# Kernel tuning notes

Measured on AMD Instinct MI355X. Metric: run time of the kernel, lower is better.

## Reference

```python
import jax, jax.numpy as jnp
import numpy as np

B, P, Q, N, D = 64, 12, 12, 1024, 64
DOW, TOD = 7, 288  # day-of-week / time-of-day one-hot depths (GMAN STEmbedding)


def setup_inputs() -> dict:
    key = jax.random.key(0)
    ks = iter(jax.random.split(key, 40))
    def g(shape, scale=0.05):
        return jax.random.normal(next(ks), shape, jnp.float32) * scale
    inp = {
        "X": jax.random.normal(next(ks), (B, P, N), jnp.float32),
        "ZC": jax.random.normal(next(ks), (B, P, 400), jnp.float32),
        "ZF": jax.random.normal(next(ks), (B, P, 1600), jnp.float32),
        "SE": g((N, D)),
        # STEmbedding FCs
        "W_se1": g((D, D)), "b_se1": jnp.zeros((D,), jnp.float32),
        "W_se2": g((D, D)), "b_se2": jnp.zeros((D,), jnp.float32),
        "W_te1": g((DOW + TOD, D)), "b_te1": jnp.zeros((D,), jnp.float32),
        "W_te2": g((D, D)), "b_te2": jnp.zeros((D,), jnp.float32),
        # FC_X_in
        "W_in1": g((1, D)), "b_in1": jnp.zeros((D,), jnp.float32),
        "W_in2": g((D, D)), "b_in2": jnp.zeros((D,), jnp.float32),
        # DCGRU layer 1 (gconv over [x||state, support@(x||state)] -> 4D input)
        "Wg1": g((4 * D, 2 * D)), "bg1": jnp.ones((2 * D,), jnp.float32),
        "Wc1": g((4 * D, D)), "bc1": jnp.zeros((D,), jnp.float32),
        # DCGRU layer 2
        "Wg2": g((4 * D, 2 * D)), "bg2": jnp.ones((2 * D,), jnp.float32),
        "Wc2": g((4 * D, D)), "bc2": jnp.zeros((D,), jnp.float32),
        # FC_X_out
        "W_o1": g((D, D)), "b_o1": jnp.zeros((D,), jnp.float32),
        "W_o2": g((D, Q)), "b_o2": jnp.zeros((Q,), jnp.float32),
        "TE": jax.random.randint(next(ks), (B, P + Q, 2), 0, 7, jnp.int32),
    }
    return inp


def _dcgru_scan(x_seq, support, Wg, bg, Wc, bc):
    """x_seq: [B,P,N,D] -> (sequence [B,P,N,D], last state [B,N,D])."""
    def gconv(x, s, W, b):
        z = jnp.concatenate([x, s], -1)                      # [B,N,2D]
        z1 = jnp.einsum('nm,bmd->bnd', support, z)           # diffusion step K=1
        return jnp.concatenate([z, z1], -1) @ W + b

    def step(state, x_t):
        ru = jax.nn.sigmoid(gconv(x_t, state, Wg, bg))       # [B,N,2D]
        r, u = jnp.split(ru, 2, axis=-1)
        c = jnp.tanh(gconv(x_t, r * state, Wc, bc))
        new = u * state + (1.0 - u) * c
        return new, new

    state0 = jnp.zeros(x_seq.shape[:1] + x_seq.shape[2:], x_seq.dtype)
    last, seq = jax.lax.scan(step, state0, jnp.swapaxes(x_seq, 0, 1))
    return jnp.swapaxes(seq, 0, 1), last


def reference(X, ZC, ZF, SE, W_se1, b_se1, W_se2, b_se2, W_te1, b_te1,
              W_te2, b_te2, W_in1, b_in1, W_in2, b_in2,
              Wg1, bg1, Wc1, bc1, Wg2, bg2, Wc2, bc2,
              W_o1, b_o1, W_o2, b_o2, TE):
    # adjacency is identity in this module; random_walk(I).T == I
    adj = jnp.eye(N, dtype=jnp.float32)
    support = (adj / jnp.sum(adj, axis=1, keepdims=True)).T

    # STEmbedding: spatial + temporal embedding
    se = jax.nn.relu(SE @ W_se1 + b_se1) @ W_se2 + b_se2                 # [N,D]
    te_oh = jnp.concatenate([
        jax.nn.one_hot(TE[..., 0], DOW, dtype=jnp.float32),
        jax.nn.one_hot(TE[..., 1], TOD, dtype=jnp.float32)], -1)        # [B,P+Q,295]
    te = jax.nn.relu(te_oh @ W_te1 + b_te1) @ W_te2 + b_te2              # [B,P+Q,D]
    STEX = (se[None, None] + te[:, :, None, :])[:, :P]                   # [B,P,N,D]

    # FC_X_in on expanded X, add STE
    Xe = X[..., None]                                                    # [B,P,N,1]
    Xe = jax.nn.relu(Xe @ W_in1 + b_in1) @ W_in2 + b_in2                 # [B,P,N,D]
    Xe = Xe + STEX

    seq1, _ = _dcgru_scan(Xe, support, Wg1, bg1, Wc1, bc1)               # [B,P,N,D]
    _, h = _dcgru_scan(seq1, support, Wg2, bg2, Wc2, bc2)                # [B,N,D]

    Y = jax.nn.relu(h @ W_o1 + b_o1) @ W_o2 + b_o2                       # [B,N,Q]
    return jnp.transpose(Y, (0, 2, 1))                                   # [B,Q,N]
```

## Files before the change

kernel.cpp:

```cpp
#include <hip/hip_runtime.h>


#define NB 1024

typedef float f32x4 __attribute__((ext_vector_type(4)));
typedef __bf16 bf16x8 __attribute__((ext_vector_type(8)));
typedef int i32x4 __attribute__((ext_vector_type(4)));
typedef unsigned int u32;
typedef unsigned short u16;

#define MFMA(a, b, c) __builtin_amdgcn_mfma_f32_16x16x32_bf16(a, b, c, 0, 0, 0)

__device__ __forceinline__ float fexp(float x) {
    return __builtin_amdgcn_exp2f(x * 1.44269504088896341f);
}
__device__ __forceinline__ float fsigmoid(float x) {
    return __builtin_amdgcn_rcpf(1.0f + fexp(-x));
}
__device__ __forceinline__ float ftanh(float x) {
    return 1.0f - 2.0f * __builtin_amdgcn_rcpf(1.0f + fexp(2.0f * x));
}

__device__ __forceinline__ u32 packf(float v) {
    u32 u = __builtin_bit_cast(u32, v);
    u32 hb = u & 0xFFFF0000u;
    float lo = v - __builtin_bit_cast(float, hb);
    return hb | (__builtin_bit_cast(u32, lo) >> 16);
}
__device__ __forceinline__ float unpackf(u32 u) {
    return __builtin_bit_cast(float, u & 0xFFFF0000u)
         + __builtin_bit_cast(float, u << 16);
}

__device__ __forceinline__ bf16x8 ldfrag(const u16* p) {
    i32x4 t = *(const i32x4*)p;
    return __builtin_bit_cast(bf16x8, t);
}
__device__ __forceinline__ bf16x8 pin(bf16x8 v) {
    i32x4 t = __builtin_bit_cast(i32x4, v);
    asm volatile("" : "+v"(t));
    return __builtin_bit_cast(bf16x8, t);
}
__device__ __forceinline__ void split8(f32x4 a0, f32x4 a1, bf16x8& hi, bf16x8& lo) {
    #pragma unroll
    for (int i = 0; i < 4; i++) {
        __bf16 h0 = (__bf16)a0[i]; hi[i] = h0;     lo[i] = (__bf16)(a0[i] - (float)h0);
        __bf16 h1 = (__bf16)a1[i]; hi[4 + i] = h1; lo[4 + i] = (__bf16)(a1[i] - (float)h1);
    }
}

#define SWZ(t) ((((t) & 3) << 3) ^ ((t) & 4) ^ (((t) & 8) << 1))
#define SW(t, k) ((t) * 64 + ((k) ^ SWZ(t)))

__device__ __forceinline__ void lda_packed(const u32* __restrict__ src, int m, int kk,
                                           bf16x8& hi, bf16x8& lo) {
    const int sk = kk ^ SWZ(m);
    i32x4 d0 = *(const i32x4*)(src + m * 64 + sk);
    i32x4 d1 = *(const i32x4*)(src + m * 64 + (sk ^ 4));
    i32x4 h, L;
    h[0] = (int)__builtin_amdgcn_perm((u32)d0[1], (u32)d0[0], 0x07060302u);
    h[1] = (int)__builtin_amdgcn_perm((u32)d0[3], (u32)d0[2], 0x07060302u);
    h[2] = (int)__builtin_amdgcn_perm((u32)d1[1], (u32)d1[0], 0x07060302u);
    h[3] = (int)__builtin_amdgcn_perm((u32)d1[3], (u32)d1[2], 0x07060302u);
    L[0] = (int)__builtin_amdgcn_perm((u32)d0[1], (u32)d0[0], 0x05040100u);
    L[1] = (int)__builtin_amdgcn_perm((u32)d0[3], (u32)d0[2], 0x05040100u);
    L[2] = (int)__builtin_amdgcn_perm((u32)d1[1], (u32)d1[0], 0x05040100u);
    L[3] = (int)__builtin_amdgcn_perm((u32)d1[3], (u32)d1[2], 0x05040100u);
    hi = __builtin_bit_cast(bf16x8, h);
    lo = __builtin_bit_cast(bf16x8, L);
}


__device__ __forceinline__ void wsplit(float v, u16* dhi, u16* dlo) {
    __bf16 h = (__bf16)v;
    __bf16 l = (__bf16)(v - (float)h);
    *dhi = __builtin_bit_cast(u16, h);
    *dlo = __builtin_bit_cast(u16, l);
}

__global__ void prep_gates(const float* __restrict__ Wg1, const float* __restrict__ Wg2,
                           u16* __restrict__ fr) {
    int i = blockIdx.x * 256 + threadIdx.x;
    if (i >= 4096) return;
    int layer = i >> 11, r = i & 2047;
    int w = r >> 9; r &= 511; int nt = r >> 8; r &= 255; int ks = r >> 6; int lane = r & 63;
    const float* Wg = layer ? Wg2 : Wg1;
    int n = lane & 15, q = lane >> 4;
    int col = nt ? (64 + w * 16 + n) : (w * 16 + n);
    u16* dst = fr + layer * 32768 + (((w * 2 + nt) * 4 + ks) * 2) * 512 + lane * 8;
    #pragma unroll
    for (int j = 0; j < 8; j++) {
        int k = ks * 32 + q * 8 + j;
        float v = Wg[k * 128 + col] + Wg[(k + 128) * 128 + col];
        wsplit(v, dst + j, dst + 512 + j);
    }
}

__global__ void prep_cand(const float* __restrict__ Wc1, const float* __restrict__ Wc2,
                          u16* __restrict__ fr) {
    int i = blockIdx.x * 256 + threadIdx.x;
    if (i >= 2048) return;
    int layer = i >> 10, r = i & 1023;
    int w = r >> 8; r &= 255; int ks = r >> 6; int lane = r & 63;
    const float* Wc = layer ? Wc2 : Wc1;
    int n = lane & 15, q = lane >> 4;
    int col = w * 16 + n;
    u16* dst = fr + 65536 + layer * 16384 + ((w * 4 + ks) * 2) * 512 + lane * 8;
    #pragma unroll
    for (int j = 0; j < 8; j++) {
        int k = ks * 32 + q * 8 + j;
        float v = Wc[k * 64 + col] + Wc[(k + 128) * 64 + col];
        wsplit(v, dst + j, dst + 512 + j);
    }
}

__global__ void prep_small(const float* __restrict__ Win2, const float* __restrict__ Wo1,
                           u16* __restrict__ fr) {
    int i = blockIdx.x * 256 + threadIdx.x;
    if (i >= 1024) return;
    int kind = i >> 9, r = i & 511;
    int w = r >> 7; r &= 127; int ks = r >> 6; int lane = r & 63;
    const float* W = kind ? Wo1 : Win2;
    int n = lane & 15, q = lane >> 4;
    int col = w * 16 + n;
    u16* dst = fr + 98304 + kind * 8192 + ((w * 2 + ks) * 2) * 512 + lane * 8;
    #pragma unroll
    for (int j = 0; j < 8; j++) {
        int k = ks * 32 + q * 8 + j;
        float v = W[k * 64 + col];
        wsplit(v, dst + j, dst + 512 + j);
    }
}

__global__ void prep_se(const float* __restrict__ SE, const float* __restrict__ W1,
                        const float* __restrict__ b1, const float* __restrict__ W2,
                        const float* __restrict__ b2, const float* __restrict__ bin2,
                        float* __restrict__ seB) {
    __shared__ float h[64];
    int n = blockIdx.x, d = threadIdx.x;
    float acc = b1[d];
    for (int k = 0; k < 64; k++) acc = fmaf(SE[n * 64 + k], W1[k * 64 + d], acc);
    h[d] = fmaxf(acc, 0.0f);
    __syncthreads();
    float acc2 = b2[d];
    for (int k = 0; k < 64; k++) acc2 = fmaf(h[k], W2[k * 64 + d], acc2);
    int nb = n >> 6, tok = n & 63;
    int mt = tok >> 4, q = (tok >> 2) & 3, r = tok & 3;
    int w = d >> 4, n16 = d & 15;
    seB[(((nb * 4 + w) * 64) + q * 16 + n16) * 16 + mt * 4 + r] = acc2 + bin2[d];
}

__global__ void prep_te(const int* __restrict__ TE, const float* __restrict__ W1,
                        const float* __restrict__ b1, const float* __restrict__ W2,
                        const float* __restrict__ b2, float* __restrict__ teo) {
    __shared__ float h[64];
    int bp = blockIdx.x;
    int b = bp / 12, p = bp - b * 12;
    int d = threadIdx.x;
    int dow = TE[(b * 24 + p) * 2 + 0];
    int tod = TE[(b * 24 + p) * 2 + 1];
    float v = W1[dow * 64 + d] + W1[(7 + tod) * 64 + d] + b1[d];
    h[d] = fmaxf(v, 0.0f);
    __syncthreads();
    float acc = b2[d];
    for (int k = 0; k < 64; k++) acc = fmaf(h[k], W2[k * 64 + d], acc);
    teo[bp * 64 + d] = acc;
}

__device__ __forceinline__ void gru_full(
    const u32* __restrict__ XIN, u32* __restrict__ S, u32* __restrict__ RS,
    const bf16x8 (&g)[16], const u16* __restrict__ frC,
    float bgr, float bgu, float bcc, int l, int col) {
    const int n16 = l & 15, q = l >> 4;
    f32x4 accR[4], accU[4], accC[4];
    #pragma unroll
    for (int mt = 0; mt < 4; mt++) {
        accR[mt] = (f32x4)0.0f; accU[mt] = (f32x4)0.0f; accC[mt] = (f32x4)0.0f;
    }
    #pragma unroll
    for (int ks = 0; ks < 2; ks++) {
        bf16x8 bhiC = ldfrag(frC + (ks * 2 + 0) * 512 + l * 8);
        bf16x8 bloC = ldfrag(frC + (ks * 2 + 1) * 512 + l * 8);
        const int kk = ks * 32 + q * 8;
        #pragma unroll
        for (int mt = 0; mt < 4; mt++) {
            bf16x8 ahi, alo;
            lda_packed(XIN, mt * 16 + n16, kk, ahi, alo);
            accR[mt] = MFMA(ahi, g[ks * 2 + 0], accR[mt]);
            accR[mt] = MFMA(alo, g[ks * 2 + 0], accR[mt]);
            accR[mt] = MFMA(ahi, g[ks * 2 + 1], accR[mt]);
            accU[mt] = MFMA(ahi, g[8 + ks * 2 + 0], accU[mt]);
            accU[mt] = MFMA(alo, g[8 + ks * 2 + 0], accU[mt]);
            accU[mt] = MFMA(ahi, g[8 + ks * 2 + 1], accU[mt]);
            accC[mt] = MFMA(ahi, bhiC, accC[mt]);
            accC[mt] = MFMA(alo, bhiC, accC[mt]);
            accC[mt] = MFMA(ahi, bloC, accC[mt]);
        }
    }
    #pragma unroll
    for (int ks = 2; ks < 4; ks++) {
        const int kk = (ks - 2) * 32 + q * 8;
        #pragma unroll
        for (int mt = 0; mt < 4; mt++) {
            bf16x8 ahi, alo;
            lda_packed(S, mt * 16 + n16, kk, ahi, alo);
            accR[mt] = MFMA(ahi, g[ks * 2 + 0], accR[mt]);
            accR[mt] = MFMA(alo, g[ks * 2 + 0], accR[mt]);
            accR[mt] = MFMA(ahi, g[ks * 2 + 1], accR[mt]);
            accU[mt] = MFMA(ahi, g[8 + ks * 2 + 0], accU[mt]);
            accU[mt] = MFMA(alo, g[8 + ks * 2 + 0], accU[mt]);
            accU[mt] = MFMA(ahi, g[8 + ks * 2 + 1], accU[mt]);
        }
    }
    float soldv[16];
    #pragma unroll
    for (int mt = 0; mt < 4; mt++)
        #pragma unroll
        for (int r = 0; r < 4; r++) {
            int tok = mt * 16 + q * 4 + r;
            int a = SW(tok, col);
            float sold = unpackf(S[a]);
            soldv[mt * 4 + r] = sold;
            RS[a] = packf(fsigmoid(accR[mt][r] + bgr) * sold);
        }
    __syncthreads();
    #pragma unroll
    for (int ks = 2; ks < 4; ks++) {
        bf16x8 bhi = ldfrag(frC + (ks * 2 + 0) * 512 + l * 8);
        bf16x8 blo = ldfrag(frC + (ks * 2 + 1) * 512 + l * 8);
        const int kk = (ks - 2) * 32 + q * 8;
        #pragma unroll
        for (int mt = 0; mt < 4; mt++) {
            bf16x8 ahi, alo;
            lda_packed(RS, mt * 16 + n16, kk, ahi, alo);
            accC[mt] = MFMA(ahi, bhi, accC[mt]);
            accC[mt] = MFMA(alo, bhi, accC[mt]);
            accC[mt] = MFMA(ahi, blo, accC[mt]);
        }
    }
    #pragma unroll
    for (int mt = 0; mt < 4; mt++)
        #pragma unroll
        for (int r = 0; r < 4; r++) {
            int tok = mt * 16 + q * 4 + r;
            int a = SW(tok, col);
            float u = fsigmoid(accU[mt][r] + bgu);
            float cnd = ftanh(accC[mt][r] + bcc);
            S[a] = packf(u * soldv[mt * 4 + r] + (1.0f - u) * cnd);
        }
    __syncthreads();
}

__global__ __launch_bounds__(256, 2) void gman_main(
    const float* __restrict__ X, const float* __restrict__ ws,
    const float* __restrict__ Win1, const float* __restrict__ bin1,
    const float* __restrict__ bg1, const float* __restrict__ bc1,
    const float* __restrict__ bg2, const float* __restrict__ bc2,
    const float* __restrict__ bo1, const float* __restrict__ Wo2,
    const float* __restrict__ bo2, float* __restrict__ out) {
    __shared__ u32 XE[4096], S1[4096], S2[4096], RS[4096];

    const int tid = threadIdx.x;
    const int l = tid & 63;
    const int w = tid >> 6;
    const int uw = __builtin_amdgcn_readfirstlane(w);
    const int n16 = l & 15, q = l >> 4;
    const int col = uw * 16 + n16;
    const int b = blockIdx.x >> 4;
    const int nb = blockIdx.x & 15;
    const int n0 = nb << 6;

    const u16* frU = (const u16*)ws;
    const u16* frG1 = frU + uw * 8192;
    const u16* frG2 = frU + 32768 + uw * 8192;
    const u16* frC1 = frU + 65536 + uw * 4096;
    const u16* frC2 = frU + 81920 + uw * 4096;
    const u16* frX  = frU + 98304 + uw * 2048;
    const u16* frH  = frU + 106496 + uw * 2048;
    const float* seQ = ws + 57344 + (((nb * 4 + uw) * 64) + l) * 16;
    const float* teo = ws + 122880;

    #pragma unroll
    for (int i = 0; i < 16; i++) { S1[tid + i * 256] = 0u; S2[tid + i * 256] = 0u; }

    bf16x8 g1[16], g2[16];
    #pragma unroll
    for (int i = 0; i < 16; i++) g1[i] = pin(ldfrag(frG1 + i * 512 + l * 8));
    #pragma unroll
    for (int i = 0; i < 16; i++) g2[i] = pin(ldfrag(frG2 + i * 512 + l * 8));

    f32x4 se_v[4];
    #pragma unroll
    for (int mt = 0; mt < 4; mt++) se_v[mt] = *(const f32x4*)(seQ + mt * 4);
    const float bg1r = bg1[col], bg1u = bg1[64 + col], bc1c = bc1[col];
    const float bg2r = bg2[col], bg2u = bg2[64 + col], bc2c = bc2[col];

    #pragma unroll 1
    for (int p = 0; p < 12; p++) {
        if (tid < 64) RS[tid] = __builtin_bit_cast(u32, X[(b * 12 + p) * NB + n0 + tid]);
        __syncthreads();
        f32x4 accX[4];
        #pragma unroll
        for (int mt = 0; mt < 4; mt++) accX[mt] = (f32x4)0.0f;
        #pragma unroll
        for (int ks = 0; ks < 2; ks++) {
            const int k0 = ks * 32 + q * 8;
            f32x4 w1a = *(const f32x4*)(Win1 + k0), w1b = *(const f32x4*)(Win1 + k0 + 4);
            f32x4 b1a = *(const f32x4*)(bin1 + k0), b1b = *(const f32x4*)(bin1 + k0 + 4);
            bf16x8 bhi = ldfrag(frX + (ks * 2 + 0) * 512 + l * 8);
            bf16x8 blo = ldfrag(frX + (ks * 2 + 1) * 512 + l * 8);
            #pragma unroll
            for (int mt = 0; mt < 4; mt++) {
                const float xm = __builtin_bit_cast(float, RS[mt * 16 + n16]);
                f32x4 h0, h1v;
                #pragma unroll
                for (int i = 0; i < 4; i++) {
                    h0[i]  = fmaxf(fmaf(xm, w1a[i], b1a[i]), 0.0f);
                    h1v[i] = fmaxf(fmaf(xm, w1b[i], b1b[i]), 0.0f);
                }
                bf16x8 ahi, alo; split8(h0, h1v, ahi, alo);
                accX[mt] = MFMA(ahi, bhi, accX[mt]);
                accX[mt] = MFMA(alo, bhi, accX[mt]);
                accX[mt] = MFMA(ahi, blo, accX[mt]);
            }
        }
        const float tev = teo[(b * 12 + p) * 64 + col];
        __syncthreads();
        #pragma unroll
        for (int mt = 0; mt < 4; mt++)
            #pragma unroll
            for (int r = 0; r < 4; r++) {
                int tok = mt * 16 + q * 4 + r;
                XE[SW(tok, col)] = packf(accX[mt][r] + se_v[mt][r] + tev);
            }
        __syncthreads();

        gru_full(XE, S1, RS, g1, frC1, bg1r, bg1u, bc1c, l, col);
        gru_full(S1, S2, RS, g2, frC2, bg2r, bg2u, bc2c, l, col);
    }

    f32x4 accH[4];
    #pragma unroll
    for (int mt = 0; mt < 4; mt++) accH[mt] = (f32x4)0.0f;
    #pragma unroll
    for (int ks = 0; ks < 2; ks++) {
        bf16x8 bhi = ldfrag(frH + (ks * 2 + 0) * 512 + l * 8);
        bf16x8 blo = ldfrag(frH + (ks * 2 + 1) * 512 + l * 8);
        const int kk = ks * 32 + q * 8;
        #pragma unroll
        for (int mt = 0; mt < 4; mt++) {
            bf16x8 ahi, alo;
            lda_packed(S2, mt * 16 + n16, kk, ahi, alo);
            accH[mt] = MFMA(ahi, bhi, accH[mt]);
            accH[mt] = MFMA(alo, bhi, accH[mt]);
            accH[mt] = MFMA(ahi, blo, accH[mt]);
        }
    }
    const float bo1c = bo1[col];
    #pragma unroll
    for (int mt = 0; mt < 4; mt++)
        #pragma unroll
        for (int r = 0; r < 4; r++) {
            int tok = mt * 16 + q * 4 + r;
            XE[SW(tok, col)] = packf(fmaxf(accH[mt][r] + bo1c, 0.0f));
        }
    __syncthreads();
    const int swzt = SWZ(l);
    float y0 = bo2[3 * uw + 0], y1 = bo2[3 * uw + 1], y2 = bo2[3 * uw + 2];
    #pragma unroll
    for (int c = 0; c < 16; c++) {
        i32x4 d = *(const i32x4*)(XE + l * 64 + c * 4);
        const int j0 = (c * 4) ^ swzt;
        #pragma unroll
        for (int e = 0; e < 4; e++) {
            float hj = unpackf((u32)d[e]);
            int j = j0 + e;
            y0 = fmaf(hj, Wo2[j * 12 + 3 * uw + 0], y0);
            y1 = fmaf(hj, Wo2[j * 12 + 3 * uw + 1], y1);
            y2 = fmaf(hj, Wo2[j * 12 + 3 * uw + 2], y2);
        }
    }
    out[(b * 12 + 3 * uw + 0) * NB + n0 + l] = y0;
    out[(b * 12 + 3 * uw + 1) * NB + n0 + l] = y1;
    out[(b * 12 + 3 * uw + 2) * NB + n0 + l] = y2;
}

extern "C" void kernel_launch(void* const* d_in, const int* in_sizes, int n_in,
                              void* d_out, int out_size, void* d_ws, size_t ws_size,
                              hipStream_t stream) {
    const float* X    = (const float*)d_in[0];
    const float* SE   = (const float*)d_in[3];
    const float* Wse1 = (const float*)d_in[4];
    const float* bse1 = (const float*)d_in[5];
    const float* Wse2 = (const float*)d_in[6];
    const float* bse2 = (const float*)d_in[7];
    const float* Wte1 = (const float*)d_in[8];
    const float* bte1 = (const float*)d_in[9];
    const float* Wte2 = (const float*)d_in[10];
    const float* bte2 = (const float*)d_in[11];
    const float* Win1 = (const float*)d_in[12];
    const float* bin1 = (const float*)d_in[13];
    const float* Win2 = (const float*)d_in[14];
    const float* bin2 = (const float*)d_in[15];
    const float* Wg1  = (const float*)d_in[16];
    const float* bg1  = (const float*)d_in[17];
    const float* Wc1  = (const float*)d_in[18];
    const float* bc1  = (const float*)d_in[19];
    const float* Wg2  = (const float*)d_in[20];
    const float* bg2  = (const float*)d_in[21];
    const float* Wc2  = (const float*)d_in[22];
    const float* bc2  = (const float*)d_in[23];
    const float* Wo1  = (const float*)d_in[24];
    const float* bo1  = (const float*)d_in[25];
    const float* Wo2  = (const float*)d_in[26];
    const float* bo2  = (const float*)d_in[27];
    const int*   TE   = (const int*)d_in[28];

    float* ws = (float*)d_ws;
    u16* fr = (u16*)ws;
    float* seB = ws + 57344;
    float* teo = ws + 122880;
    float* out = (float*)d_out;

    prep_gates<<<16, 256, 0, stream>>>(Wg1, Wg2, fr);
    prep_cand<<<8, 256, 0, stream>>>(Wc1, Wc2, fr);
    prep_small<<<4, 256, 0, stream>>>(Win2, Wo1, fr);
    prep_se<<<1024, 64, 0, stream>>>(SE, Wse1, bse1, Wse2, bse2, bin2, seB);
    prep_te<<<768, 64, 0, stream>>>(TE, Wte1, bte1, Wte2, bte2, teo);
    gman_main<<<1024, 256, 0, stream>>>(X, ws, Win1, bin1, bg1, bc1, bg2, bc2,
                                        bo1, Wo2, bo2, out);
}
```

Baseline: 574.8 us.

## Stream gate weights from memory and drop RS buffer to fit three blocks per CU

Gate weight fragments are no longer held in registers for the whole kernel. They are reloaded from global memory inside each GRU step, and old state values are re-read from LDS instead of being kept in registers. The separate RS shared buffer is removed by aliasing it onto XE, with an extra barrier in the first layer, and launch bounds are raised to 3 blocks per CU. This trades repeated global/L2 weight loads and one more sync for lower register and LDS use, aiming for higher occupancy to hide latency.

```diff
diff --git a/kernel.cpp b/kernel.cpp
--- a/kernel.cpp
+++ b/kernel.cpp
@@ -34,11 +34,6 @@
 
 __device__ __forceinline__ bf16x8 ldfrag(const u16* p) {
     i32x4 t = *(const i32x4*)p;
-    return __builtin_bit_cast(bf16x8, t);
-}
-__device__ __forceinline__ bf16x8 pin(bf16x8 v) {
-    i32x4 t = __builtin_bit_cast(i32x4, v);
-    asm volatile("" : "+v"(t));
     return __builtin_bit_cast(bf16x8, t);
 }
 __device__ __forceinline__ void split8(f32x4 a0, f32x4 a1, bf16x8& hi, bf16x8& lo) {
@@ -167,9 +162,10 @@
     teo[bp * 64 + d] = acc;
 }
 
+template <bool ALIAS>
 __device__ __forceinline__ void gru_full(
     const u32* __restrict__ XIN, u32* __restrict__ S, u32* __restrict__ RS,
-    const bf16x8 (&g)[16], const u16* __restrict__ frC,
+    const u16* __restrict__ frG, const u16* __restrict__ frC,
     float bgr, float bgu, float bcc, int l, int col) {
     const int n16 = l & 15, q = l >> 4;
     f32x4 accR[4], accU[4], accC[4];
@@ -179,6 +175,10 @@
     }
     #pragma unroll
     for (int ks = 0; ks < 2; ks++) {
+        bf16x8 gRh = ldfrag(frG + (ks * 2 + 0) * 512 + l * 8);
+        bf16x8 gRl = ldfrag(frG + (ks * 2 + 1) * 512 + l * 8);
+        bf16x8 gUh = ldfrag(frG + (8 + ks * 2 + 0) * 512 + l * 8);
+        bf16x8 gUl = ldfrag(frG + (8 + ks * 2 + 1) * 512 + l * 8);
         bf16x8 bhiC = ldfrag(frC + (ks * 2 + 0) * 512 + l * 8);
         bf16x8 bloC = ldfrag(frC + (ks * 2 + 1) * 512 + l * 8);
         const int kk = ks * 32 + q * 8;
@@ -186,12 +186,12 @@
         for (int mt = 0; mt < 4; mt++) {
             bf16x8 ahi, alo;
             lda_packed(XIN, mt * 16 + n16, kk, ahi, alo);
-            accR[mt] = MFMA(ahi, g[ks * 2 + 0], accR[mt]);
-            accR[mt] = MFMA(alo, g[ks * 2 + 0], accR[mt]);
-            accR[mt] = MFMA(ahi, g[ks * 2 + 1], accR[mt]);
-            accU[mt] = MFMA(ahi, g[8 + ks * 2 + 0], accU[mt]);
-            accU[mt] = MFMA(alo, g[8 + ks * 2 + 0], accU[mt]);
-            accU[mt] = MFMA(ahi, g[8 + ks * 2 + 1], accU[mt]);
+            accR[mt] = MFMA(ahi, gRh, accR[mt]);
+            accR[mt] = MFMA(alo, gRh, accR[mt]);
+            accR[mt] = MFMA(ahi, gRl, accR[mt]);
+            accU[mt] = MFMA(ahi, gUh, accU[mt]);
+            accU[mt] = MFMA(alo, gUh, accU[mt]);
+            accU[mt] = MFMA(ahi, gUl, accU[mt]);
             accC[mt] = MFMA(ahi, bhiC, accC[mt]);
             accC[mt] = MFMA(alo, bhiC, accC[mt]);
             accC[mt] = MFMA(ahi, bloC, accC[mt]);
@@ -199,29 +199,31 @@
     }
     #pragma unroll
     for (int ks = 2; ks < 4; ks++) {
+        bf16x8 gRh = ldfrag(frG + (ks * 2 + 0) * 512 + l * 8);
+        bf16x8 gRl = ldfrag(frG + (ks * 2 + 1) * 512 + l * 8);
+        bf16x8 gUh = ldfrag(frG + (8 + ks * 2 + 0) * 512 + l * 8);
+        bf16x8 gUl = ldfrag(frG + (8 + ks * 2 + 1) * 512 + l * 8);
         const int kk = (ks - 2) * 32 + q * 8;
         #pragma unroll
         for (int mt = 0; mt < 4; mt++) {
             bf16x8 ahi, alo;
             lda_packed(S, mt * 16 + n16, kk, ahi, alo);
-            accR[mt] = MFMA(ahi, g[ks * 2 + 0], accR[mt]);
-            accR[mt] = MFMA(alo, g[ks * 2 + 0], accR[mt]);
-            accR[mt] = MFMA(ahi, g[ks * 2 + 1], accR[mt]);
-            accU[mt] = MFMA(ahi, g[8 + ks * 2 + 0], accU[mt]);
-            accU[mt] = MFMA(alo, g[8 + ks * 2 + 0], accU[mt]);
-            accU[mt] = MFMA(ahi, g[8 + ks * 2 + 1], accU[mt]);
-        }
-    }
-    float soldv[16];
+            accR[mt] = MFMA(ahi, gRh, accR[mt]);
+            accR[mt] = MFMA(alo, gRh, accR[mt]);
+            accR[mt] = MFMA(ahi, gRl, accR[mt]);
+            accU[mt] = MFMA(ahi, gUh, accU[mt]);
+            accU[mt] = MFMA(alo, gUh, accU[mt]);
+            accU[mt] = MFMA(ahi, gUl, accU[mt]);
+        }
+    }
+    if (ALIAS) __syncthreads();
     #pragma unroll
     for (int mt = 0; mt < 4; mt++)
         #pragma unroll
         for (int r = 0; r < 4; r++) {
             int tok = mt * 16 + q * 4 + r;
             int a = SW(tok, col);
-            float sold = unpackf(S[a]);
-            soldv[mt * 4 + r] = sold;
-            RS[a] = packf(fsigmoid(accR[mt][r] + bgr) * sold);
+            RS[a] = packf(fsigmoid(accR[mt][r] + bgr) * unpackf(S[a]));
         }
     __syncthreads();
     #pragma unroll
@@ -246,19 +248,20 @@
             int a = SW(tok, col);
             float u = fsigmoid(accU[mt][r] + bgu);
             float cnd = ftanh(accC[mt][r] + bcc);
-            S[a] = packf(u * soldv[mt * 4 + r] + (1.0f - u) * cnd);
+            float sold = unpackf(S[a]);
+            S[a] = packf(u * sold + (1.0f - u) * cnd);
         }
     __syncthreads();
 }
 
-__global__ __launch_bounds__(256, 2) void gman_main(
+__global__ __launch_bounds__(256, 3) void gman_main(
     const float* __restrict__ X, const float* __restrict__ ws,
     const float* __restrict__ Win1, const float* __restrict__ bin1,
     const float* __restrict__ bg1, const float* __restrict__ bc1,
     const float* __restrict__ bg2, const float* __restrict__ bc2,
     const float* __restrict__ bo1, const float* __restrict__ Wo2,
     const float* __restrict__ bo2, float* __restrict__ out) {
-    __shared__ u32 XE[4096], S1[4096], S2[4096], RS[4096];
+    __shared__ u32 XE[4096], S1[4096], S2[4096];
 
     const int tid = threadIdx.x;
     const int l = tid & 63;
@@ -283,12 +286,6 @@
     #pragma unroll
     for (int i = 0; i < 16; i++) { S1[tid + i * 256] = 0u; S2[tid + i * 256] = 0u; }
 
-    bf16x8 g1[16], g2[16];
-    #pragma unroll
-    for (int i = 0; i < 16; i++) g1[i] = pin(ldfrag(frG1 + i * 512 + l * 8));
-    #pragma unroll
-    for (int i = 0; i < 16; i++) g2[i] = pin(ldfrag(frG2 + i * 512 + l * 8));
-
     f32x4 se_v[4];
     #pragma unroll
     for (int mt = 0; mt < 4; mt++) se_v[mt] = *(const f32x4*)(seQ + mt * 4);
@@ -297,7 +294,7 @@
 
     #pragma unroll 1
     for (int p = 0; p < 12; p++) {
-        if (tid < 64) RS[tid] = __builtin_bit_cast(u32, X[(b * 12 + p) * NB + n0 + tid]);
+        if (tid < 64) XE[tid] = __builtin_bit_cast(u32, X[(b * 12 + p) * NB + n0 + tid]);
         __syncthreads();
         f32x4 accX[4];
         #pragma unroll
@@ -311,7 +308,7 @@
             bf16x8 blo = ldfrag(frX + (ks * 2 + 1) * 512 + l * 8);
             #pragma unroll
             for (int mt = 0; mt < 4; mt++) {
-                const float xm = __builtin_bit_cast(float, RS[mt * 16 + n16]);
+                const float xm = __builtin_bit_cast(float, XE[mt * 16 + n16]);
                 f32x4 h0, h1v;
                 #pragma unroll
                 for (int i = 0; i < 4; i++) {
@@ -335,8 +332,8 @@
             }
         __syncthreads();
 
-        gru_full(XE, S1, RS, g1, frC1, bg1r, bg1u, bc1c, l, col);
-        gru_full(S1, S2, RS, g2, frC2, bg2r, bg2u, bc2c, l, col);
+        gru_full<true >(XE, S1, XE, frG1, frC1, bg1r, bg1u, bc1c, l, col);
+        gru_full<false>(S1, S2, XE, frG2, frC2, bg2r, bg2u, bc2c, l, col);
     }
 
     f32x4 accH[4];
```

Result: slower. 1.453 ms (+152.9%).
